# Performance work log

Measured on AMD Instinct MI355X. Metric: run time of the kernel, lower is better.

## Reference

```python
import jax, jax.numpy as jnp
import numpy as np

N_NODES = 50000
N_EDGES = 800000
BATCH = 16384
DNN_IN, DNN_H = 256, 64
GNN_IN, GNN_H = 64, 64
COMBO = DNN_H + GNN_H          # 128
MID = round(COMBO / 2)         # 64
BN_EPS = 1e-5


def gcn_conv(x, edge_index, W, b):
    """PyG GCNConv: symmetric norm with self-loops. x:[N,Fin] -> [N,Fout]."""
    n = x.shape[0]
    h = x @ W                                      # [N, Fout]
    row, col = edge_index[0], edge_index[1]
    ones = jnp.ones(edge_index.shape[1], dtype=x.dtype)
    deg = jax.ops.segment_sum(ones, col, num_segments=n) + 1.0   # +1 self-loop
    dis = jax.lax.rsqrt(deg)                       # deg^{-1/2}
    norm = dis[row] * dis[col]                     # [E]
    agg = jax.ops.segment_sum(norm[:, None] * h[row], col, num_segments=n)
    # self-loop contribution: norm = dis[i]*dis[i]
    return agg + (dis * dis)[:, None] * h + b


def setup_inputs() -> dict:
    key = jax.random.key(0)
    ks = jax.random.split(key, 16)
    s = 0.05
    return {
        "x1": jax.random.normal(ks[0], (BATCH, DNN_IN), jnp.float32),
        "x2": jax.random.normal(ks[1], (N_NODES, GNN_IN), jnp.float32),
        "edge_index": jax.random.randint(ks[2], (2, N_EDGES), 0, N_NODES, dtype=jnp.int64),
        "dnn_W": jax.random.normal(ks[3], (DNN_IN, DNN_H), jnp.float32) * s,
        "dnn_b": jnp.zeros((DNN_H,), jnp.float32),
        "bn_gamma": jnp.ones((DNN_H,), jnp.float32),
        "bn_beta": jnp.zeros((DNN_H,), jnp.float32),
        "gcn1_W": jax.random.normal(ks[4], (GNN_IN, GNN_H), jnp.float32) * s,
        "gcn1_b": jnp.zeros((GNN_H,), jnp.float32),
        "gcn2_W": jax.random.normal(ks[5], (GNN_H, GNN_H), jnp.float32) * s,
        "gcn2_b": jnp.zeros((GNN_H,), jnp.float32),
        "fc1_W": jax.random.normal(ks[6], (COMBO, MID), jnp.float32) * s,
        "fc1_b": jnp.zeros((MID,), jnp.float32),
        "fc2_W": jax.random.normal(ks[7], (MID, 1), jnp.float32) * s,
        "fc2_b": jnp.zeros((1,), jnp.float32),
    }


def reference(x1, x2, edge_index, dnn_W, dnn_b, bn_gamma, bn_beta,
              gcn1_W, gcn1_b, gcn2_W, gcn2_b, fc1_W, fc1_b, fc2_W, fc2_b):
    # DNN branch: Linear -> BatchNorm1d (batch stats, training mode) -> ReLU
    h = x1 @ dnn_W + dnn_b                          # [B, 64]
    mu = jnp.mean(h, axis=0)
    var = jnp.var(h, axis=0)
    hn = (h - mu) * jax.lax.rsqrt(var + BN_EPS) * bn_gamma + bn_beta
    dnn_emb = jax.nn.relu(hn)                       # [B, 64]

    # GNN branch: GCNConv -> ReLU -> GCNConv -> mean over nodes
    g = jax.nn.relu(gcn_conv(x2, edge_index, gcn1_W, gcn1_b))
    g = gcn_conv(g, edge_index, gcn2_W, gcn2_b)
    gnn_emb = jnp.mean(g, axis=0)                   # [64]

    # concat (gnn_emb broadcast over batch) + small MLP
    gnn_b = jnp.broadcast_to(gnn_emb, (x1.shape[0], gnn_emb.shape[0]))
    x = jnp.concatenate([dnn_emb, gnn_b], axis=1)   # [B, 128]
    x = x @ fc1_W + fc1_b
    x = x @ fc2_W + fc2_b
    return x                                        # [B, 1]
```

## Files before the change

### kernel.cpp

```cpp
#include <hip/hip_runtime.h>
#include <hip/hip_fp16.h>

#define NN 50000
#define NE 800000
#define NB 16384

#define NBKT 784
#define BCAP 1280
#define CAPL 8
#define P1B  256
#define DNNB 256

typedef unsigned int uint;
typedef unsigned short ushort;

__device__ __forceinline__ uint pack2h(float a, float b) {
    return (uint)__half_as_ushort(__float2half_rn(a)) |
           ((uint)__half_as_ushort(__float2half_rn(b)) << 16);
}
__device__ __forceinline__ float h2f(ushort u) {
    return __half2float(__ushort_as_half(u));
}

__global__ void zero_kernel(int* __restrict__ p, int n)
{
    for (int i = threadIdx.x; i < n; i += 256) p[i] = 0;
}

struct BinSh {
    uint st[NBKT * CAPL];
    int lc[NBKT];
};
union MegaSh {
    BinSh b;
    float xs[64 * 65];
};

__global__ __launch_bounds__(512) void mega(const int* __restrict__ ei,
    uint* __restrict__ bufC, uint* __restrict__ bufR,
    int* __restrict__ gcurC, int* __restrict__ gcurR,
    const float* __restrict__ X1, const float* __restrict__ Wd,
    float* __restrict__ H, float* __restrict__ bnsum,
    float* __restrict__ bnsumsq,
    const float* __restrict__ X2, const float* __restrict__ W1,
    ushort* __restrict__ Hh)
{
    __shared__ MegaSh sh;
    const int tid = threadIdx.x;
    const int lane = tid & 63;
    const int wv = __builtin_amdgcn_readfirstlane(tid >> 6);

    if (blockIdx.x < P1B) {
        BinSh& B = sh.b;
        const int per = (NE + P1B - 1) / P1B;
        const int lo = blockIdx.x * per;
        const int hi = (lo + per < NE) ? lo + per : NE;
        for (int i = tid; i < NBKT; i += 512) B.lc[i] = 0;
        __syncthreads();
        for (int e = lo + tid; e < hi; e += 512) {
            int r = ei[e], c = ei[NE + e];
            uint ent = ((uint)r << 6) | (uint)(c & 63);
            int b = c >> 6;
            int pos = atomicAdd(&B.lc[b], 1);
            if (pos < CAPL) B.st[b * CAPL + pos] = ent;
            else { int gp = atomicAdd(&gcurC[b], 1); bufC[(size_t)b * BCAP + gp] = ent; }
        }
        __syncthreads();
        for (int base = wv * 8; base < NBKT; base += 64) {
            int wb = base + (lane >> 3);
            int idx = lane & 7;
            int n = B.lc[wb]; if (n > CAPL) n = CAPL;
            int gb = 0;
            if (idx == 0 && n > 0) gb = atomicAdd(&gcurC[wb], n);
            gb = __shfl(gb, lane & 56);
            if (idx < n) bufC[(size_t)wb * BCAP + gb + idx] = B.st[wb * CAPL + idx];
        }
        __syncthreads();
        for (int i = tid; i < NBKT; i += 512) B.lc[i] = 0;
        __syncthreads();
        for (int e = lo + tid; e < hi; e += 512) {
            int r = ei[e], c = ei[NE + e];
            uint ent = ((uint)(r & 63) << 16) | (uint)c;
            int rb = r >> 6;
            int pos = atomicAdd(&B.lc[rb], 1);
            if (pos < CAPL) B.st[rb * CAPL + pos] = ent;
            else { int gp = atomicAdd(&gcurR[rb], 1); bufR[(size_t)rb * BCAP + gp] = ent; }
        }
        __syncthreads();
        for (int base = wv * 8; base < NBKT; base += 64) {
            int wb = base + (lane >> 3);
            int idx = lane & 7;
            int n = B.lc[wb]; if (n > CAPL) n = CAPL;
            int gb = 0;
            if (idx == 0 && n > 0) gb = atomicAdd(&gcurR[wb], n);
            gb = __shfl(gb, lane & 56);
            if (idx < n) bufR[(size_t)wb * BCAP + gb + idx] = B.st[wb * CAPL + idx];
        }
        return;
    }

    if (blockIdx.x < P1B + DNNB) {
        float* xs = sh.xs;
        const int c0 = wv * 8;
        const int row0 = (blockIdx.x - P1B) * 64;
        float acc[8];
#pragma unroll
        for (int j = 0; j < 8; ++j) acc[j] = 0.f;
#pragma unroll 1
        for (int chunk = 0; chunk < 4; ++chunk) {
            if (chunk) __syncthreads();
            for (int i = tid; i < 4096; i += 512) {
                int r = i >> 6, k = i & 63;
                xs[r * 65 + k] = X1[(size_t)(row0 + r) * 256 + chunk * 64 + k];
            }
            __syncthreads();
            const float* xrow = xs + lane * 65;
#pragma unroll
            for (int k4 = 0; k4 < 16; ++k4) {
                float x0 = xrow[4 * k4 + 0];
                float x1 = xrow[4 * k4 + 1];
                float x2 = xrow[4 * k4 + 2];
                float x3 = xrow[4 * k4 + 3];
                const float* wr = Wd + (size_t)(chunk * 64 + 4 * k4) * 64 + c0;
#pragma unroll
                for (int j = 0; j < 8; ++j) {
                    float a = acc[j];
                    a = fmaf(x0, wr[j],       a);
                    a = fmaf(x1, wr[64 + j],  a);
                    a = fmaf(x2, wr[128 + j], a);
                    a = fmaf(x3, wr[192 + j], a);
                    acc[j] = a;
                }
            }
        }
        __syncthreads();
#pragma unroll
        for (int j = 0; j < 8; ++j) xs[lane * 65 + c0 + j] = acc[j];
        __syncthreads();
        float s = 0.f, q = 0.f;
        for (int i = tid; i < 4096; i += 512) {
            int r = i >> 6, c = i & 63;
            float v = xs[r * 65 + c];
            H[(size_t)(row0 + r) * 64 + c] = v;
            s += v; q += v * v;
        }
        __syncthreads();
        float* red = xs;
        red[tid] = s; red[512 + tid] = q;
        __syncthreads();
        if (tid < 64) {
            float ss = 0.f, qq = 0.f;
#pragma unroll
            for (int gidx = 0; gidx < 8; ++gidx) {
                ss += red[gidx * 64 + tid];
                qq += red[512 + gidx * 64 + tid];
            }
            atomicAdd(&bnsum[tid], ss);
            atomicAdd(&bnsumsq[tid], qq);
        }
        return;
    }

    {
        float* xs = sh.xs;
        const int c0 = wv * 8;
        const int row0 = (blockIdx.x - P1B - DNNB) * 64;
        float acc[8];
#pragma unroll
        for (int j = 0; j < 8; ++j) acc[j] = 0.f;
        if (row0 + 64 <= NN) {
            for (int i = tid; i < 4096; i += 512) {
                int r = i >> 6, k = i & 63;
                xs[r * 65 + k] = X2[(size_t)(row0 + r) * 64 + k];
            }
        } else {
            for (int i = tid; i < 4096; i += 512) {
                int r = i >> 6, k = i & 63;
                xs[r * 65 + k] = (row0 + r < NN)
                               ? X2[(size_t)(row0 + r) * 64 + k] : 0.f;
            }
        }
        __syncthreads();
        const float* xrow = xs + lane * 65;
#pragma unroll
        for (int k4 = 0; k4 < 16; ++k4) {
            float x0 = xrow[4 * k4 + 0];
            float x1 = xrow[4 * k4 + 1];
            float x2 = xrow[4 * k4 + 2];
            float x3 = xrow[4 * k4 + 3];
            const float* wr = W1 + (size_t)(4 * k4) * 64 + c0;
#pragma unroll
            for (int j = 0; j < 8; ++j) {
                float a = acc[j];
                a = fmaf(x0, wr[j],       a);
                a = fmaf(x1, wr[64 + j],  a);
                a = fmaf(x2, wr[128 + j], a);
                a = fmaf(x3, wr[192 + j], a);
                acc[j] = a;
            }
        }
        __syncthreads();
#pragma unroll
        for (int j = 0; j < 8; ++j) xs[lane * 65 + c0 + j] = acc[j];
        __syncthreads();
        for (int i = tid; i < 2048; i += 512) {
            int r = i >> 5, cp = (i & 31) * 2;
            int row = row0 + r;
            if (row < NN) {
                uint v = pack2h(xs[r * 65 + cp], xs[r * 65 + cp + 1]);
                *reinterpret_cast<uint*>(Hh + (size_t)row * 64 + cp) = v;
            }
        }
    }
}

__global__ __launch_bounds__(256) void cnt_dis_scale(const uint* __restrict__ bufC,
    const int* __restrict__ gcurC, ushort* __restrict__ Hh,
    float* __restrict__ dis, int* __restrict__ cnth)
{
    __shared__ int hist[64];
    __shared__ float disS[64];
    const int tid = threadIdx.x, bb = blockIdx.x;
    const int row0 = bb * 64;
    if (tid < 64) hist[tid] = 0;
    __syncthreads();
    const int n = gcurC[bb];
    const uint* src = bufC + (size_t)bb * BCAP;
    for (int i = tid; i < n; i += 256) atomicAdd(&hist[src[i] & 63], 1);
    __syncthreads();
    if (tid < 64) {
        int c = row0 + tid;
        cnth[row0 + tid] = hist[tid];
        float d = rsqrtf((float)hist[tid] + 1.0f);
        disS[tid] = d;
        if (c < NN) dis[c] = d;
    }
    __syncthreads();
    for (int i = tid; i < 2048; i += 256) {
        int r = i >> 5, cp = (i & 31) * 2;
        int row = row0 + r;
        if (row < NN) {
            uint* p = reinterpret_cast<uint*>(Hh + (size_t)row * 64 + cp);
            uint v = *p;
            float d = disS[r];
            *p = pack2h(d * h2f((ushort)(v & 0xffffu)),
                        d * h2f((ushort)(v >> 16)));
        }
    }
}

__global__ __launch_bounds__(512) void gather_pass(const uint* __restrict__ bufC,
    const int* __restrict__ gcurC, const int* __restrict__ cnth,
    const uint* __restrict__ bufR, const int* __restrict__ gcurR,
    const float* __restrict__ dis, const ushort* __restrict__ hs,
    const float* __restrict__ b1, float* __restrict__ svec)
{
    __shared__ int sorted[BCAP];
    __shared__ int cntS[64], offsS[64], curS[64];
    __shared__ float w[64];
    __shared__ float red[8][64];
    const int tid = threadIdx.x;
    const int lane = tid & 63;
    const int wv = __builtin_amdgcn_readfirstlane(tid >> 6);
    const int bb = blockIdx.x;
    const int g4 = lane >> 4;
    const int l16 = lane & 15;
    if (tid < 64) {
        w[tid] = 0.f;
        int v = cnth[bb * 64 + tid];
        cntS[tid] = v;
        int s = v;
#pragma unroll
        for (int o = 1; o < 64; o <<= 1) {
            int u = __shfl_up(s, o);
            if (lane >= o) s += u;
        }
        offsS[tid] = s - v;
        curS[tid] = s - v;
    }
    __syncthreads();
    const int n2 = gcurR[bb];
    const uint* srcR = bufR + (size_t)bb * BCAP;
    for (int i = tid; i < n2; i += 512) {
        uint e = srcR[i];
        atomicAdd(&w[e >> 16], dis[e & 0xffffu]);
    }
    const int n = gcurC[bb];
    const uint* src = bufC + (size_t)bb * BCAP;
    for (int i = tid; i < n; i += 512) {
        uint e = src[i];
        int p = atomicAdd(&curS[e & 63u], 1);
        sorted[p] = (int)(e >> 6);
    }
    __syncthreads();
    float sacc0 = 0.f, sacc1 = 0.f, sacc2 = 0.f, sacc3 = 0.f;
    const float4 blv = *reinterpret_cast<const float4*>(b1 + (l16 << 2));
#pragma unroll 1
    for (int t = 0; t < 8; ++t) {
        const int nd = wv * 8 + t;
        const int lo = offsS[nd], hi2 = lo + cntS[nd];
        float a0 = 0.f, a1 = 0.f, a2 = 0.f, a3 = 0.f;
        for (int e = lo; e < hi2; e += 8) {
            int i0 = e + g4;
            int i1 = e + 4 + g4;
            int j0 = (i0 < hi2) ? i0 : hi2 - 1;
            int j1 = (i1 < hi2) ? i1 : hi2 - 1;
            float s0 = (i0 < hi2) ? 1.f : 0.f;
            float s1 = (i1 < hi2) ? 1.f : 0.f;
            int r0 = sorted[j0];
            int r1 = sorted[j1];
            uint2 v0 = *reinterpret_cast<const uint2*>(hs + ((size_t)r0 << 6) + (l16 << 2));
            uint2 v1 = *reinterpret_cast<const uint2*>(hs + ((size_t)r1 << 6) + (l16 << 2));
            a0 = fmaf(s0, h2f((ushort)(v0.x & 0xffffu)), a0);
            a1 = fmaf(s0, h2f((ushort)(v0.x >> 16)),     a1);
            a2 = fmaf(s0, h2f((ushort)(v0.y & 0xffffu)), a2);
            a3 = fmaf(s0, h2f((ushort)(v0.y >> 16)),     a3);
            a0 = fmaf(s1, h2f((ushort)(v1.x & 0xffffu)), a0);
            a1 = fmaf(s1, h2f((ushort)(v1.x >> 16)),     a1);
            a2 = fmaf(s1, h2f((ushort)(v1.y & 0xffffu)), a2);
            a3 = fmaf(s1, h2f((ushort)(v1.y >> 16)),     a3);
        }
        a0 += __shfl_xor(a0, 16); a0 += __shfl_xor(a0, 32);
        a1 += __shfl_xor(a1, 16); a1 += __shfl_xor(a1, 32);
        a2 += __shfl_xor(a2, 16); a2 += __shfl_xor(a2, 32);
        a3 += __shfl_xor(a3, 16); a3 += __shfl_xor(a3, 32);
        const int c = bb * 64 + nd;
        if (c < NN) {
            float d = dis[c];
            float coef = fmaf(d, w[nd], d * d);
            uint2 sv = *reinterpret_cast<const uint2*>(hs + ((size_t)c << 6) + (l16 << 2));
            float g0 = fmaf(d, a0 + h2f((ushort)(sv.x & 0xffffu)), blv.x);
            float g1 = fmaf(d, a1 + h2f((ushort)(sv.x >> 16)),     blv.y);
            float g2 = fmaf(d, a2 + h2f((ushort)(sv.y & 0xffffu)), blv.z);
            float g3 = fmaf(d, a3 + h2f((ushort)(sv.y >> 16)),     blv.w);
            sacc0 = fmaf(coef, fmaxf(g0, 0.f), sacc0);
            sacc1 = fmaf(coef, fmaxf(g1, 0.f), sacc1);
            sacc2 = fmaf(coef, fmaxf(g2, 0.f), sacc2);
            sacc3 = fmaf(coef, fmaxf(g3, 0.f), sacc3);
        }
    }
    if (g4 == 0) {
        red[wv][(l16 << 2) + 0] = sacc0;
        red[wv][(l16 << 2) + 1] = sacc1;
        red[wv][(l16 << 2) + 2] = sacc2;
        red[wv][(l16 << 2) + 3] = sacc3;
    }
    __syncthreads();
    if (wv == 0) {
        float s = ((red[0][lane] + red[1][lane]) + (red[2][lane] + red[3][lane])) +
                  ((red[4][lane] + red[5][lane]) + (red[6][lane] + red[7][lane]));
        atomicAdd(&svec[lane], s);
    }
}

__global__ __launch_bounds__(256) void out_final(const float* __restrict__ H,
    const float* __restrict__ bnsum, const float* __restrict__ bnsumsq,
    const float* __restrict__ gamma, const float* __restrict__ beta,
    const float* __restrict__ svec, const float* __restrict__ g2W,
    const float* __restrict__ g2b, const float* __restrict__ fc1W,
    const float* __restrict__ fc1b, const float* __restrict__ fc2W,
    const float* __restrict__ fc2b, float* __restrict__ out)
{
    __shared__ float scaleS[64], shiftS[64], vdnnS[64];
    __shared__ float consS;
    const int tid = threadIdx.x;
    const int lane = tid & 63;
    const int grp = tid >> 6;
    if (tid < 64) {
        int j = tid;
        float mu = bnsum[j] * (1.0f / NB);
        float var = bnsumsq[j] * (1.0f / NB) - mu * mu;
        float sc = rsqrtf(var + 1e-5f) * gamma[j];
        scaleS[j] = sc;
        shiftS[j] = beta[j] - mu * sc;
        float ge = 0.f;
        for (int k = 0; k < 64; ++k) ge += svec[k] * g2W[k * 64 + j];
        ge = ge * (1.0f / NN) + g2b[j];
        float vd = 0.f, vg = 0.f;
        for (int k = 0; k < 64; ++k) {
            vd += fc1W[j * 64 + k] * fc2W[k];
            vg += fc1W[(64 + j) * 64 + k] * fc2W[k];
        }
        vdnnS[j] = vd;
        float part = ge * vg + fc1b[j] * fc2W[j];
#pragma unroll
        for (int o = 32; o > 0; o >>= 1) part += __shfl_down(part, o);
        if (j == 0) consS = part + fc2b[0];
    }
    __syncthreads();
    const float sc = scaleS[lane], sh = shiftS[lane], vd = vdnnS[lane];
    const float C = consS;
#pragma unroll 1
    for (int t = 0; t < 8; ++t) {
        int i = blockIdx.x * 32 + grp * 8 + t;
        float x = H[(size_t)i * 64 + lane] * sc + sh;
        x = fmaxf(x, 0.f) * vd;
#pragma unroll
        for (int o = 32; o > 0; o >>= 1) x += __shfl_down(x, o);
        if (lane == 0) out[i] = x + C;
    }
}

extern "C" void kernel_launch(void* const* d_in, const int* in_sizes, int n_in,
                              void* d_out, int out_size, void* d_ws, size_t ws_size,
                              hipStream_t stream)
{
    const float* x1    = (const float*)d_in[0];
    const float* x2    = (const float*)d_in[1];
    const int*   ei    = (const int*)d_in[2];
    const float* dnnW  = (const float*)d_in[3];
    const float* gamma = (const float*)d_in[5];
    const float* beta  = (const float*)d_in[6];
    const float* g1W   = (const float*)d_in[7];
    const float* g1b   = (const float*)d_in[8];
    const float* g2W   = (const float*)d_in[9];
    const float* g2b   = (const float*)d_in[10];
    const float* fc1W  = (const float*)d_in[11];
    const float* fc1b  = (const float*)d_in[12];
    const float* fc2W  = (const float*)d_in[13];
    const float* fc2b  = (const float*)d_in[14];

    float* ws      = (float*)d_ws;
    ushort* h1h    = (ushort*)ws;
    float* hdnn    = ws + 1605632;
    float* dis     = hdnn + 1048576;
    int*   cnth    = (int*)(dis + 50176 + 25088);
    uint*  bufC    = (uint*)(cnth + 50176);
    uint*  bufR    = bufC + NBKT * BCAP;
    int*   gcurC   = (int*)(bufR + NBKT * BCAP);
    int*   gcurR   = gcurC + NBKT;
    float* bnsum   = (float*)(gcurR + NBKT);
    float* bnsumsq = bnsum + 64;
    float* svec    = bnsumsq + 64;

    zero_kernel<<<1, 256, 0, stream>>>(gcurC, NBKT * 2 + 192);

    mega<<<P1B + DNNB + NBKT, 512, 0, stream>>>(ei, bufC, bufR, gcurC, gcurR,
                                                x1, dnnW, hdnn, bnsum, bnsumsq,
                                                x2, g1W, h1h);
    cnt_dis_scale<<<NBKT, 256, 0, stream>>>(bufC, gcurC, h1h, dis, cnth);
    gather_pass<<<NBKT, 512, 0, stream>>>(bufC, gcurC, cnth, bufR, gcurR,
                                          dis, h1h, g1b, svec);
    out_final<<<512, 256, 0, stream>>>(hdnn, bnsum, bnsumsq, gamma, beta, svec,
                                       g2W, g2b, fc1W, fc1b, fc2W, fc2b,
                                       (float*)d_out);
}
```

Measured before the change: 103.6 us.

## Compute degrees via global atomics in mega kernel and drop cnt_dis_scale pass

```diff
diff --git a/kernel.cpp b/kernel.cpp
--- a/kernel.cpp
+++ b/kernel.cpp
@@ -8,6 +8,7 @@
 #define NBKT 784
 #define BCAP 1280
 #define CAPL 8
+#define CNTB 128
 #define P1B  256
 #define DNNB 256
 
@@ -24,7 +25,8 @@
 
 __global__ void zero_kernel(int* __restrict__ p, int n)
 {
-    for (int i = threadIdx.x; i < n; i += 256) p[i] = 0;
+    for (int i = blockIdx.x * 256 + threadIdx.x; i < n; i += gridDim.x * 256)
+        p[i] = 0;
 }
 
 struct BinSh {
@@ -39,6 +41,7 @@
 __global__ __launch_bounds__(512) void mega(const int* __restrict__ ei,
     uint* __restrict__ bufC, uint* __restrict__ bufR,
     int* __restrict__ gcurC, int* __restrict__ gcurR,
+    int* __restrict__ cntg,
     const float* __restrict__ X1, const float* __restrict__ Wd,
     float* __restrict__ H, float* __restrict__ bnsum,
     float* __restrict__ bnsumsq,
@@ -50,10 +53,17 @@
     const int lane = tid & 63;
     const int wv = __builtin_amdgcn_readfirstlane(tid >> 6);
 
-    if (blockIdx.x < P1B) {
+    if (blockIdx.x < CNTB) {
+        for (int e = blockIdx.x * 512 + tid; e < NE; e += CNTB * 512)
+            atomicAdd(&cntg[ei[NE + e]], 1);
+        return;
+    }
+
+    if (blockIdx.x < CNTB + P1B) {
         BinSh& B = sh.b;
+        const int bid = blockIdx.x - CNTB;
         const int per = (NE + P1B - 1) / P1B;
-        const int lo = blockIdx.x * per;
+        const int lo = bid * per;
         const int hi = (lo + per < NE) ? lo + per : NE;
         for (int i = tid; i < NBKT; i += 512) B.lc[i] = 0;
         __syncthreads();
@@ -99,10 +109,10 @@
         return;
     }
 
-    if (blockIdx.x < P1B + DNNB) {
+    if (blockIdx.x < CNTB + P1B + DNNB) {
         float* xs = sh.xs;
         const int c0 = wv * 8;
-        const int row0 = (blockIdx.x - P1B) * 64;
+        const int row0 = (blockIdx.x - CNTB - P1B) * 64;
         float acc[8];
 #pragma unroll
         for (int j = 0; j < 8; ++j) acc[j] = 0.f;
@@ -164,7 +174,7 @@
     {
         float* xs = sh.xs;
         const int c0 = wv * 8;
-        const int row0 = (blockIdx.x - P1B - DNNB) * 64;
+        const int row0 = (blockIdx.x - CNTB - P1B - DNNB) * 64;
         float acc[8];
 #pragma unroll
         for (int j = 0; j < 8; ++j) acc[j] = 0.f;
@@ -214,50 +224,15 @@
     }
 }
 
-__global__ __launch_bounds__(256) void cnt_dis_scale(const uint* __restrict__ bufC,
-    const int* __restrict__ gcurC, ushort* __restrict__ Hh,
-    float* __restrict__ dis, int* __restrict__ cnth)
-{
-    __shared__ int hist[64];
-    __shared__ float disS[64];
-    const int tid = threadIdx.x, bb = blockIdx.x;
-    const int row0 = bb * 64;
-    if (tid < 64) hist[tid] = 0;
-    __syncthreads();
-    const int n = gcurC[bb];
-    const uint* src = bufC + (size_t)bb * BCAP;
-    for (int i = tid; i < n; i += 256) atomicAdd(&hist[src[i] & 63], 1);
-    __syncthreads();
-    if (tid < 64) {
-        int c = row0 + tid;
-        cnth[row0 + tid] = hist[tid];
-        float d = rsqrtf((float)hist[tid] + 1.0f);
-        disS[tid] = d;
-        if (c < NN) dis[c] = d;
-    }
-    __syncthreads();
-    for (int i = tid; i < 2048; i += 256) {
-        int r = i >> 5, cp = (i & 31) * 2;
-        int row = row0 + r;
-        if (row < NN) {
-            uint* p = reinterpret_cast<uint*>(Hh + (size_t)row * 64 + cp);
-            uint v = *p;
-            float d = disS[r];
-            *p = pack2h(d * h2f((ushort)(v & 0xffffu)),
-                        d * h2f((ushort)(v >> 16)));
-        }
-    }
-}
-
 __global__ __launch_bounds__(512) void gather_pass(const uint* __restrict__ bufC,
-    const int* __restrict__ gcurC, const int* __restrict__ cnth,
+    const int* __restrict__ gcurC, const int* __restrict__ cntg,
     const uint* __restrict__ bufR, const int* __restrict__ gcurR,
-    const float* __restrict__ dis, const ushort* __restrict__ hs,
-    const float* __restrict__ b1, float* __restrict__ svec)
+    const ushort* __restrict__ hs, const float* __restrict__ b1,
+    float* __restrict__ svec)
 {
     __shared__ int sorted[BCAP];
     __shared__ int cntS[64], offsS[64], curS[64];
-    __shared__ float w[64];
+    __shared__ float w[64], disS[64];
     __shared__ float red[8][64];
     const int tid = threadIdx.x;
     const int lane = tid & 63;
@@ -267,8 +242,9 @@
     const int l16 = lane & 15;
     if (tid < 64) {
         w[tid] = 0.f;
-        int v = cnth[bb * 64 + tid];
+        int v = cntg[bb * 64 + tid];
         cntS[tid] = v;
+        disS[tid] = rsqrtf((float)v + 1.0f);
         int s = v;
 #pragma unroll
         for (int o = 1; o < 64; o <<= 1) {
@@ -283,7 +259,8 @@
     const uint* srcR = bufR + (size_t)bb * BCAP;
     for (int i = tid; i < n2; i += 512) {
         uint e = srcR[i];
-        atomicAdd(&w[e >> 16], dis[e & 0xffffu]);
+        float dc = rsqrtf((float)cntg[e & 0xffffu] + 1.0f);
+        atomicAdd(&w[e >> 16], dc);
     }
     const int n = gcurC[bb];
     const uint* src = bufC + (size_t)bb * BCAP;
@@ -305,20 +282,22 @@
             int i1 = e + 4 + g4;
             int j0 = (i0 < hi2) ? i0 : hi2 - 1;
             int j1 = (i1 < hi2) ? i1 : hi2 - 1;
-            float s0 = (i0 < hi2) ? 1.f : 0.f;
-            float s1 = (i1 < hi2) ? 1.f : 0.f;
+            float m0 = (i0 < hi2) ? 1.f : 0.f;
+            float m1 = (i1 < hi2) ? 1.f : 0.f;
             int r0 = sorted[j0];
             int r1 = sorted[j1];
+            float sd0 = m0 * rsqrtf((float)cntg[r0] + 1.0f);
+            float sd1 = m1 * rsqrtf((float)cntg[r1] + 1.0f);
             uint2 v0 = *reinterpret_cast<const uint2*>(hs + ((size_t)r0 << 6) + (l16 << 2));
             uint2 v1 = *reinterpret_cast<const uint2*>(hs + ((size_t)r1 << 6) + (l16 << 2));
-            a0 = fmaf(s0, h2f((ushort)(v0.x & 0xffffu)), a0);
-            a1 = fmaf(s0, h2f((ushort)(v0.x >> 16)),     a1);
-            a2 = fmaf(s0, h2f((ushort)(v0.y & 0xffffu)), a2);
-            a3 = fmaf(s0, h2f((ushort)(v0.y >> 16)),     a3);
-            a0 = fmaf(s1, h2f((ushort)(v1.x & 0xffffu)), a0);
-            a1 = fmaf(s1, h2f((ushort)(v1.x >> 16)),     a1);
-            a2 = fmaf(s1, h2f((ushort)(v1.y & 0xffffu)), a2);
-            a3 = fmaf(s1, h2f((ushort)(v1.y >> 16)),     a3);
+            a0 = fmaf(sd0, h2f((ushort)(v0.x & 0xffffu)), a0);
+            a1 = fmaf(sd0, h2f((ushort)(v0.x >> 16)),     a1);
+            a2 = fmaf(sd0, h2f((ushort)(v0.y & 0xffffu)), a2);
+            a3 = fmaf(sd0, h2f((ushort)(v0.y >> 16)),     a3);
+            a0 = fmaf(sd1, h2f((ushort)(v1.x & 0xffffu)), a0);
+            a1 = fmaf(sd1, h2f((ushort)(v1.x >> 16)),     a1);
+            a2 = fmaf(sd1, h2f((ushort)(v1.y & 0xffffu)), a2);
+            a3 = fmaf(sd1, h2f((ushort)(v1.y >> 16)),     a3);
         }
         a0 += __shfl_xor(a0, 16); a0 += __shfl_xor(a0, 32);
         a1 += __shfl_xor(a1, 16); a1 += __shfl_xor(a1, 32);
@@ -326,13 +305,13 @@
         a3 += __shfl_xor(a3, 16); a3 += __shfl_xor(a3, 32);
         const int c = bb * 64 + nd;
         if (c < NN) {
-            float d = dis[c];
+            float d = disS[nd];
             float coef = fmaf(d, w[nd], d * d);
             uint2 sv = *reinterpret_cast<const uint2*>(hs + ((size_t)c << 6) + (l16 << 2));
-            float g0 = fmaf(d, a0 + h2f((ushort)(sv.x & 0xffffu)), blv.x);
-            float g1 = fmaf(d, a1 + h2f((ushort)(sv.x >> 16)),     blv.y);
-            float g2 = fmaf(d, a2 + h2f((ushort)(sv.y & 0xffffu)), blv.z);
-            float g3 = fmaf(d, a3 + h2f((ushort)(sv.y >> 16)),     blv.w);
+            float g0 = fmaf(d, fmaf(d, h2f((ushort)(sv.x & 0xffffu)), a0), blv.x);
+            float g1 = fmaf(d, fmaf(d, h2f((ushort)(sv.x >> 16)),     a1), blv.y);
+            float g2 = fmaf(d, fmaf(d, h2f((ushort)(sv.y & 0xffffu)), a2), blv.z);
+            float g3 = fmaf(d, fmaf(d, h2f((ushort)(sv.y >> 16)),     a3), blv.w);
             sacc0 = fmaf(coef, fmaxf(g0, 0.f), sacc0);
             sacc1 = fmaf(coef, fmaxf(g1, 0.f), sacc1);
             sacc2 = fmaf(coef, fmaxf(g2, 0.f), sacc2);
@@ -423,24 +402,23 @@
     float* ws      = (float*)d_ws;
     ushort* h1h    = (ushort*)ws;
     float* hdnn    = ws + 1605632;
-    float* dis     = hdnn + 1048576;
-    int*   cnth    = (int*)(dis + 50176 + 25088);
-    uint*  bufC    = (uint*)(cnth + 50176);
+    uint*  bufC    = (uint*)(hdnn + 1048576);
     uint*  bufR    = bufC + NBKT * BCAP;
     int*   gcurC   = (int*)(bufR + NBKT * BCAP);
     int*   gcurR   = gcurC + NBKT;
     float* bnsum   = (float*)(gcurR + NBKT);
     float* bnsumsq = bnsum + 64;
     float* svec    = bnsumsq + 64;
-
-    zero_kernel<<<1, 256, 0, stream>>>(gcurC, NBKT * 2 + 192);
-
-    mega<<<P1B + DNNB + NBKT, 512, 0, stream>>>(ei, bufC, bufR, gcurC, gcurR,
-                                                x1, dnnW, hdnn, bnsum, bnsumsq,
-                                                x2, g1W, h1h);
-    cnt_dis_scale<<<NBKT, 256, 0, stream>>>(bufC, gcurC, h1h, dis, cnth);
-    gather_pass<<<NBKT, 512, 0, stream>>>(bufC, gcurC, cnth, bufR, gcurR,
-                                          dis, h1h, g1b, svec);
+    int*   cntg    = (int*)(svec + 64);
+
+    const int ZN = NBKT * 2 + 192 + 50176;
+    zero_kernel<<<64, 256, 0, stream>>>(gcurC, ZN);
+
+    mega<<<CNTB + P1B + DNNB + NBKT, 512, 0, stream>>>(
+        ei, bufC, bufR, gcurC, gcurR, cntg,
+        x1, dnnW, hdnn, bnsum, bnsumsq, x2, g1W, h1h);
+    gather_pass<<<NBKT, 512, 0, stream>>>(bufC, gcurC, cntg, bufR, gcurR,
+                                          h1h, g1b, svec);
     out_final<<<512, 256, 0, stream>>>(hdnn, bnsum, bnsumsq, gamma, beta, svec,
                                        g2W, g2b, fc1W, fc1b, fc2W, fc2b,
                                        (float*)d_out);
```

Result: slower. 117.7 us (+13.7%).
